# Performance work log

Hardware: AMD Instinct MI355X
Metric: run time of the kernel (lower is better)

Reference implementation:

```python
import jax, jax.numpy as jnp
import numpy as np

VOCAB = 100000
N_BLOCKS = 4
BLOCK_SIZES = [(25000, 64), (25000, 128), (25000, 256), (25000, 512)]
OUT_DIM = 512
B, L = 8, 2048


def setup_inputs() -> dict:
    key = jax.random.key(0)
    ks = jax.random.split(key, 2 * N_BLOCKS + 1)
    src = jax.random.randint(ks[0], (B, L), 0, VOCAB, dtype=jnp.int64 if jax.config.jax_enable_x64 else jnp.int32).astype(jnp.int32)
    # deterministic assignment: vocab idx -> block idx % 4, local row idx // 4
    idx = jnp.arange(VOCAB, dtype=jnp.int32)
    block_assignment = idx % N_BLOCKS
    local_assignment = idx // N_BLOCKS
    inp = {"src": src, "block_assignment": block_assignment, "local_assignment": local_assignment}
    for b, (num, size) in enumerate(BLOCK_SIZES):
        # embedding_initializer: normal_ (std=1); transformer_initializer: xavier_uniform_
        inp[f"block{b}"] = jax.random.normal(ks[1 + b], (num, size), dtype=jnp.float32)
        bound = np.sqrt(6.0 / (size + OUT_DIM))
        inp[f"trans{b}"] = jax.random.uniform(ks[1 + N_BLOCKS + b], (size, OUT_DIM), dtype=jnp.float32, minval=-bound, maxval=bound)
    return inp


def reference(src, block_assignment, local_assignment, block0, block1, block2, block3, trans0, trans1, trans2, trans3):
    blocks = [block0, block1, block2, block3]
    transformers = [trans0, trans1, trans2, trans3]
    ba = block_assignment[src]  # [B, L] which block each token routes to
    la = local_assignment[src]  # [B, L] row within that block's table
    out = jnp.zeros(src.shape + (OUT_DIM,), dtype=block0.dtype)
    for b in range(N_BLOCKS):
        tbl, tr = blocks[b], transformers[b]
        safe_la = jnp.clip(la, 0, tbl.shape[0] - 1)
        vec = tbl[safe_la]                      # [B, L, size_b] gather
        ob = jnp.einsum('bls,sd->bld', vec, tr)  # per-block transform
        out = jnp.where((ba == b)[..., None], ob, out)
    return out
```

## Files before the change

### kernel.cpp

```cpp
#include <hip/hip_runtime.h>
#include <stdint.h>


#define OUT_DIM 512
#define TOKBITS 14
#define TOKMASK ((1 << TOKBITS) - 1)

typedef __attribute__((ext_vector_type(8))) short short8;
typedef __attribute__((ext_vector_type(4))) float floatx4;

__device__ __forceinline__ uint16_t f2bf(float f) {
    union { float f; uint32_t u; } x; x.f = f;
    uint32_t u = x.u + 0x7FFF + ((x.u >> 16) & 1);
    return (uint16_t)(u >> 16);
}

__global__ __launch_bounds__(256) void prep_bsw(
    const float* __restrict__ t0, const float* __restrict__ t1,
    const float* __restrict__ t2, const float* __restrict__ t3,
    uint16_t* __restrict__ bsw, int* __restrict__ counts) {
    if (blockIdx.x == 0 && threadIdx.x < 4) counts[threadIdx.x] = 0;
    int gid = blockIdx.x * 256 + threadIdx.x;
    const float* tr; int S; int f; uint16_t* dst;
    if (gid < 4096)       { tr = t0; S = 64;  f = gid;         dst = bsw; }
    else if (gid < 12288) { tr = t1; S = 128; f = gid - 4096;  dst = bsw + 64 * 512; }
    else if (gid < 28672) { tr = t2; S = 256; f = gid - 12288; dst = bsw + (64 + 128) * 512; }
    else if (gid < 61440) { tr = t3; S = 512; f = gid - 28672; dst = bsw + (64 + 128 + 256) * 512; }
    else return;
    const int lane = f & 63, rest = f >> 6;
    const int ksteps = S >> 5;
    const int ks = rest & (ksteps - 1), ntile = rest / ksteps;
    const int quad = lane >> 4, nl = lane & 15;
    const int n = ntile * 16 + nl, k0 = ks * 32 + quad * 8;
    short8 v;
#pragma unroll
    for (int j = 0; j < 8; ++j) v[j] = (short)f2bf(tr[(k0 + j) * OUT_DIM + n]);
    *(short8*)(dst + (size_t)f * 8) = v;
}

__global__ __launch_bounds__(256) void scatter_kernel(
    const int* __restrict__ src, const int* __restrict__ ba, const int* __restrict__ la,
    int* __restrict__ counts, int* __restrict__ lists, int n_tokens, int stride) {
    __shared__ int lc[4], gbase[4];
    const int tid = (int)threadIdx.x;
    if (tid < 4) lc[tid] = 0;
    __syncthreads();
    const int t = blockIdx.x * 256 + tid;
    int b = 0, pos = 0, packed = 0;
    const bool active = (t < n_tokens);
    if (active) {
        int v = src[t];
        b = ba[v];
        int r = min(max(la[v], 0), 24999);
        packed = t | (r << TOKBITS);
        pos = atomicAdd(&lc[b], 1);
    }
    __syncthreads();
    if (tid < 4) gbase[tid] = atomicAdd(&counts[tid], lc[tid]);
    __syncthreads();
    if (active) lists[b * stride + gbase[b] + pos] = packed;
}

template <int S>
__device__ __forceinline__ void gemm3_body(
    const float* __restrict__ tbl, const uint16_t* __restrict__ bswb,
    const int* __restrict__ list, int n, int g, int nhalf,
    float* __restrict__ out, uint16_t* lds) {
    const int base = g * 16;
    const int m = min(16, n - base);
    const int tid = (int)threadIdx.x;
    constexpr int SP = S + 8;
    constexpr int CH = S / 4;
    constexpr int KS = S / 32;

    for (int i = tid; i < 16 * CH; i += 256) {
        const int row = i / CH, c = i & (CH - 1);
        float4 v = make_float4(0.f, 0.f, 0.f, 0.f);
        if (row < m) {
            const int r = list[base + row] >> TOKBITS;
            v = ((const float4*)(tbl + (size_t)r * S))[c];
        }
        const uint32_t lo = ((uint32_t)f2bf(v.y) << 16) | f2bf(v.x);
        const uint32_t hi = ((uint32_t)f2bf(v.w) << 16) | f2bf(v.z);
        *(uint2*)(lds + row * SP + c * 4) = make_uint2(lo, hi);
    }
    __syncthreads();

    const int wave = tid >> 6, lane = tid & 63;
    const int quad = lane >> 4, ml = lane & 15;
    const int ntb = nhalf * 16 + wave * 4;

    floatx4 acc[4];
#pragma unroll
    for (int nt = 0; nt < 4; ++nt) acc[nt] = (floatx4)0.f;

    const short8* B = (const short8*)bswb;
#pragma unroll
    for (int ks = 0; ks < KS; ++ks) {
        const short8 a = *(const short8*)(lds + ml * SP + ks * 32 + quad * 8);
#pragma unroll
        for (int nt = 0; nt < 4; ++nt) {
            const short8 bf = B[(size_t)((ntb + nt) * KS + ks) * 64 + lane];
            acc[nt] = __builtin_amdgcn_mfma_f32_16x16x32_bf16(a, bf, acc[nt], 0, 0, 0);
        }
    }

#pragma unroll
    for (int r = 0; r < 4; ++r) {
        const int tokidx = quad * 4 + r;
        if (tokidx < m) {
            const int t = list[base + tokidx] & TOKMASK;
            float* op = out + (size_t)t * OUT_DIM + nhalf * 256 + wave * 64 + ml;
#pragma unroll
            for (int nt = 0; nt < 4; ++nt) op[nt * 16] = acc[nt][r];
        }
    }
}

__global__ __launch_bounds__(256, 6) void gemm_mfma_v3(
    const float* __restrict__ b0, const float* __restrict__ b1,
    const float* __restrict__ b2, const float* __restrict__ b3,
    const uint16_t* __restrict__ bsw,
    const int* __restrict__ lists, const int* __restrict__ counts,
    float* __restrict__ out, int stride) {
    extern __shared__ uint16_t lds[];
    const int c0 = counts[0], c1 = counts[1], c2 = counts[2], c3 = counts[3];
    const int g0 = (c0 + 15) >> 4, g1 = (c1 + 15) >> 4, g2 = (c2 + 15) >> 4, g3 = (c3 + 15) >> 4;
    const int flat = (int)blockIdx.x;
    const int nhalf = (int)blockIdx.y;
    if (flat >= g0 + g1 + g2 + g3) return;
    if (flat < g0) {
        gemm3_body<64 >(b0, bsw, lists + 0L * stride, c0, flat, nhalf, out, lds);
    } else if (flat < g0 + g1) {
        gemm3_body<128>(b1, bsw + 64 * 512, lists + 1L * stride, c1, flat - g0, nhalf, out, lds);
    } else if (flat < g0 + g1 + g2) {
        gemm3_body<256>(b2, bsw + (64 + 128) * 512, lists + 2L * stride, c2, flat - g0 - g1, nhalf, out, lds);
    } else {
        gemm3_body<512>(b3, bsw + (64 + 128 + 256) * 512, lists + 3L * stride, c3, flat - g0 - g1 - g2, nhalf, out, lds);
    }
}

#define TOK 16
template <int S>
__device__ __forceinline__ void gemm_body(const float* __restrict__ tbl,
                                          const float* __restrict__ tr,
                                          const int* __restrict__ list,
                                          const int* __restrict__ counts,
                                          float* __restrict__ out,
                                          float* lvec, int b) {
    const int n = counts[b];
    const int base = (int)blockIdx.x * TOK;
    if (base >= n) return;
    const int m = min(TOK, n - base);
    const int tid = (int)threadIdx.x;
    const int nch = TOK * S / 4;
    for (int i = tid; i < nch; i += 256) {
        const int tok = i / (S / 4), c = i % (S / 4);
        float4 v = make_float4(0.f, 0.f, 0.f, 0.f);
        if (tok < m) {
            const int row = list[base + tok] >> TOKBITS;
            v = ((const float4*)(tbl + (size_t)row * S))[c];
        }
        ((float4*)lvec)[i] = v;
    }
    __syncthreads();
    float acc0[TOK], acc1[TOK];
#pragma unroll
    for (int tok = 0; tok < TOK; ++tok) { acc0[tok] = 0.f; acc1[tok] = 0.f; }
#pragma unroll 2
    for (int k = 0; k < S; k += 4) {
        float w00 = tr[(k + 0) * OUT_DIM + tid], w01 = tr[(k + 0) * OUT_DIM + tid + 256];
        float w10 = tr[(k + 1) * OUT_DIM + tid], w11 = tr[(k + 1) * OUT_DIM + tid + 256];
        float w20 = tr[(k + 2) * OUT_DIM + tid], w21 = tr[(k + 2) * OUT_DIM + tid + 256];
        float w30 = tr[(k + 3) * OUT_DIM + tid], w31 = tr[(k + 3) * OUT_DIM + tid + 256];
#pragma unroll
        for (int tok = 0; tok < TOK; ++tok) {
            float4 tv = *(const float4*)&lvec[tok * S + k];
            acc0[tok] += tv.x * w00 + tv.y * w10 + tv.z * w20 + tv.w * w30;
            acc1[tok] += tv.x * w01 + tv.y * w11 + tv.z * w21 + tv.w * w31;
        }
    }
    for (int tok = 0; tok < m; ++tok) {
        const int t = list[base + tok] & TOKMASK;
        out[(size_t)t * OUT_DIM + tid] = acc0[tok];
        out[(size_t)t * OUT_DIM + tid + 256] = acc1[tok];
    }
}

__global__ __launch_bounds__(256) void gemm_all(
    const float* __restrict__ b0, const float* __restrict__ b1,
    const float* __restrict__ b2, const float* __restrict__ b3,
    const float* __restrict__ t0, const float* __restrict__ t1,
    const float* __restrict__ t2, const float* __restrict__ t3,
    const int* __restrict__ lists, const int* __restrict__ counts,
    float* __restrict__ out, int stride) {
    extern __shared__ float lvec[];
    switch ((int)blockIdx.y) {
        case 0: gemm_body<64 >(b0, t0, lists + 0L * stride, counts, out, lvec, 0); break;
        case 1: gemm_body<128>(b1, t1, lists + 1L * stride, counts, out, lvec, 1); break;
        case 2: gemm_body<256>(b2, t2, lists + 2L * stride, counts, out, lvec, 2); break;
        case 3: gemm_body<512>(b3, t3, lists + 3L * stride, counts, out, lvec, 3); break;
    }
}

__global__ __launch_bounds__(256) void per_token_kernel(
    const int* __restrict__ src, const int* __restrict__ ba, const int* __restrict__ la,
    const float* __restrict__ b0, const float* __restrict__ b1,
    const float* __restrict__ b2, const float* __restrict__ b3,
    const float* __restrict__ t0, const float* __restrict__ t1,
    const float* __restrict__ t2, const float* __restrict__ t3,
    float* __restrict__ out) {
    __shared__ float lvec[OUT_DIM];
    const int t = (int)blockIdx.x, tid = (int)threadIdx.x;
    const int v = src[t];
    const int b = ba[v];
    int r = min(max(la[v], 0), 24999);
    const float* tbl; const float* tr; int S;
    switch (b) {
        case 0: tbl = b0; tr = t0; S = 64;  break;
        case 1: tbl = b1; tr = t1; S = 128; break;
        case 2: tbl = b2; tr = t2; S = 256; break;
        default: tbl = b3; tr = t3; S = 512; break;
    }
    if (tid < S / 4) ((float4*)lvec)[tid] = ((const float4*)(tbl + (size_t)r * S))[tid];
    __syncthreads();
    float acc0 = 0.f, acc1 = 0.f;
    for (int k = 0; k < S; ++k) {
        float x = lvec[k];
        acc0 += x * tr[k * OUT_DIM + tid];
        acc1 += x * tr[k * OUT_DIM + tid + 256];
    }
    out[(size_t)t * OUT_DIM + tid] = acc0;
    out[(size_t)t * OUT_DIM + tid + 256] = acc1;
}

extern "C" void kernel_launch(void* const* d_in, const int* in_sizes, int n_in,
                              void* d_out, int out_size, void* d_ws, size_t ws_size,
                              hipStream_t stream) {
    const int*   src = (const int*)d_in[0];
    const int*   ba  = (const int*)d_in[1];
    const int*   la  = (const int*)d_in[2];
    const float* b0  = (const float*)d_in[3];
    const float* t0  = (const float*)d_in[4];
    const float* b1  = (const float*)d_in[5];
    const float* t1  = (const float*)d_in[6];
    const float* b2  = (const float*)d_in[7];
    const float* t2  = (const float*)d_in[8];
    const float* b3  = (const float*)d_in[9];
    const float* t3  = (const float*)d_in[10];
    float* out = (float*)d_out;

    const int n_tokens = in_sizes[0];
    const size_t off_lists = 16;
    const size_t off_bsw   = off_lists + (size_t)4 * n_tokens * sizeof(int);
    const size_t bsw_bytes = (size_t)(64 + 128 + 256 + 512) * 512 * sizeof(uint16_t);
    const size_t need_full = off_bsw + bsw_bytes;
    const size_t need_fp32 = off_bsw;

    if (d_ws != nullptr && ws_size >= need_full) {
        int* counts   = (int*)d_ws;
        int* lists    = (int*)((char*)d_ws + off_lists);
        uint16_t* bsw = (uint16_t*)((char*)d_ws + off_bsw);
        prep_bsw<<<240, 256, 0, stream>>>(t0, t1, t2, t3, bsw, counts);
        scatter_kernel<<<(n_tokens + 255) / 256, 256, 0, stream>>>(
            src, ba, la, counts, lists, n_tokens, n_tokens);
        const int gmax = (n_tokens + 15) / 16 + 3;
        dim3 grid(gmax, 2);
        gemm_mfma_v3<<<grid, 256, 16 * (512 + 8) * sizeof(uint16_t), stream>>>(
            b0, b1, b2, b3, bsw, lists, counts, out, n_tokens);
    } else if (d_ws != nullptr && ws_size >= need_fp32) {
        int* counts = (int*)d_ws;
        int* lists  = (int*)((char*)d_ws + off_lists);
        hipMemsetAsync(d_ws, 0, 16, stream);
        scatter_kernel<<<(n_tokens + 255) / 256, 256, 0, stream>>>(
            src, ba, la, counts, lists, n_tokens, n_tokens);
        const int groups = (n_tokens + TOK - 1) / TOK;
        dim3 grid(groups, 4);
        gemm_all<<<grid, 256, TOK * OUT_DIM * sizeof(float), stream>>>(
            b0, b1, b2, b3, t0, t1, t2, t3, lists, counts, out, n_tokens);
    } else {
        per_token_kernel<<<n_tokens, 256, 0, stream>>>(
            src, ba, la, b0, b1, b2, b3, t0, t1, t2, t3, out);
    }
}
```

Measured before the change: 156.5 us.

## Fuse weight prep with token scatter and tile two M-tiles for small blocks

Merges the weight swizzle and the token scatter into one launch, with counts zeroed by a memset instead of inside the kernel. The MFMA GEMM now processes 32 tokens per workgroup for the 64- and 128-wide blocks, so each B fragment load feeds two MFMAs. Outputs are written with nontemporal stores. The trade-offs are an extra memset call, more registers (launch bound lowered to 5 waves), and the LDS size must still cover 32 rows of the smaller blocks.

```diff
diff --git a/kernel.cpp b/kernel.cpp
--- a/kernel.cpp
+++ b/kernel.cpp
@@ -15,29 +15,144 @@
     return (uint16_t)(u >> 16);
 }
 
-__global__ __launch_bounds__(256) void prep_bsw(
+__global__ __launch_bounds__(256) void prep_scatter(
     const float* __restrict__ t0, const float* __restrict__ t1,
     const float* __restrict__ t2, const float* __restrict__ t3,
-    uint16_t* __restrict__ bsw, int* __restrict__ counts) {
-    if (blockIdx.x == 0 && threadIdx.x < 4) counts[threadIdx.x] = 0;
-    int gid = blockIdx.x * 256 + threadIdx.x;
-    const float* tr; int S; int f; uint16_t* dst;
-    if (gid < 4096)       { tr = t0; S = 64;  f = gid;         dst = bsw; }
-    else if (gid < 12288) { tr = t1; S = 128; f = gid - 4096;  dst = bsw + 64 * 512; }
-    else if (gid < 28672) { tr = t2; S = 256; f = gid - 12288; dst = bsw + (64 + 128) * 512; }
-    else if (gid < 61440) { tr = t3; S = 512; f = gid - 28672; dst = bsw + (64 + 128 + 256) * 512; }
-    else return;
-    const int lane = f & 63, rest = f >> 6;
-    const int ksteps = S >> 5;
-    const int ks = rest & (ksteps - 1), ntile = rest / ksteps;
-    const int quad = lane >> 4, nl = lane & 15;
-    const int n = ntile * 16 + nl, k0 = ks * 32 + quad * 8;
-    short8 v;
-#pragma unroll
-    for (int j = 0; j < 8; ++j) v[j] = (short)f2bf(tr[(k0 + j) * OUT_DIM + n]);
-    *(short8*)(dst + (size_t)f * 8) = v;
-}
-
+    uint16_t* __restrict__ bsw,
+    const int* __restrict__ src, const int* __restrict__ ba, const int* __restrict__ la,
+    int* __restrict__ counts, int* __restrict__ lists, int n_tokens, int stride) {
+    const int bx = (int)blockIdx.x;
+    const int tid = (int)threadIdx.x;
+    if (bx < 240) {
+        int gid = bx * 256 + tid;
+        const float* tr; int S; int f; uint16_t* dst;
+        if (gid < 4096)       { tr = t0; S = 64;  f = gid;         dst = bsw; }
+        else if (gid < 12288) { tr = t1; S = 128; f = gid - 4096;  dst = bsw + 64 * 512; }
+        else if (gid < 28672) { tr = t2; S = 256; f = gid - 12288; dst = bsw + (64 + 128) * 512; }
+        else                  { tr = t3; S = 512; f = gid - 28672; dst = bsw + (64 + 128 + 256) * 512; }
+        const int lane = f & 63, rest = f >> 6;
+        const int ksteps = S >> 5;
+        const int ks = rest & (ksteps - 1), ntile = rest / ksteps;
+        const int quad = lane >> 4, nl = lane & 15;
+        const int n = ntile * 16 + nl, k0 = ks * 32 + quad * 8;
+        short8 v;
+#pragma unroll
+        for (int j = 0; j < 8; ++j) v[j] = (short)f2bf(tr[(k0 + j) * OUT_DIM + n]);
+        *(short8*)(dst + (size_t)f * 8) = v;
+    } else {
+        __shared__ int lc[4], gbase[4];
+        if (tid < 4) lc[tid] = 0;
+        __syncthreads();
+        const int t = (bx - 240) * 256 + tid;
+        int b = 0, pos = 0, packed = 0;
+        const bool active = (t < n_tokens);
+        if (active) {
+            int v = src[t];
+            b = ba[v];
+            int r = min(max(la[v], 0), 24999);
+            packed = t | (r << TOKBITS);
+            pos = atomicAdd(&lc[b], 1);
+        }
+        __syncthreads();
+        if (tid < 4) gbase[tid] = atomicAdd(&counts[tid], lc[tid]);
+        __syncthreads();
+        if (active) lists[b * stride + gbase[b] + pos] = packed;
+    }
+}
+
+template <int S, int MT>
+__device__ __forceinline__ void gemm4_body(
+    const float* __restrict__ tbl, const uint16_t* __restrict__ bswb,
+    const int* __restrict__ list, int n, int g, int nhalf,
+    float* __restrict__ out, uint16_t* lds) {
+    constexpr int ROWS = MT * 16;
+    const int base = g * ROWS;
+    const int m = min(ROWS, n - base);
+    const int tid = (int)threadIdx.x;
+    constexpr int SP = S + 8;
+    constexpr int CH = S / 4;
+    constexpr int KS = S / 32;
+
+    for (int i = tid; i < ROWS * CH; i += 256) {
+        const int row = i / CH, c = i & (CH - 1);
+        float4 v = make_float4(0.f, 0.f, 0.f, 0.f);
+        if (row < m) {
+            const int r = list[base + row] >> TOKBITS;
+            v = ((const float4*)(tbl + (size_t)r * S))[c];
+        }
+        const uint32_t lo = ((uint32_t)f2bf(v.y) << 16) | f2bf(v.x);
+        const uint32_t hi = ((uint32_t)f2bf(v.w) << 16) | f2bf(v.z);
+        *(uint2*)(lds + row * SP + c * 4) = make_uint2(lo, hi);
+    }
+    __syncthreads();
+
+    const int wave = tid >> 6, lane = tid & 63;
+    const int quad = lane >> 4, ml = lane & 15;
+    const int ntb = nhalf * 16 + wave * 4;
+
+    floatx4 acc[MT][4];
+#pragma unroll
+    for (int mt = 0; mt < MT; ++mt)
+#pragma unroll
+        for (int nt = 0; nt < 4; ++nt) acc[mt][nt] = (floatx4)0.f;
+
+    const short8* B = (const short8*)bswb;
+#pragma unroll
+    for (int ks = 0; ks < KS; ++ks) {
+        short8 a[MT];
+#pragma unroll
+        for (int mt = 0; mt < MT; ++mt)
+            a[mt] = *(const short8*)(lds + (mt * 16 + ml) * SP + ks * 32 + quad * 8);
+#pragma unroll
+        for (int nt = 0; nt < 4; ++nt) {
+            const short8 bf = B[(size_t)((ntb + nt) * KS + ks) * 64 + lane];
+#pragma unroll
+            for (int mt = 0; mt < MT; ++mt)
+                acc[mt][nt] = __builtin_amdgcn_mfma_f32_16x16x32_bf16(a[mt], bf, acc[mt][nt], 0, 0, 0);
+        }
+    }
+
+#pragma unroll
+    for (int mt = 0; mt < MT; ++mt) {
+#pragma unroll
+        for (int r = 0; r < 4; ++r) {
+            const int tokidx = mt * 16 + quad * 4 + r;
+            if (tokidx < m) {
+                const int t = list[base + tokidx] & TOKMASK;
+                float* op = out + (size_t)t * OUT_DIM + nhalf * 256 + wave * 64 + ml;
+#pragma unroll
+                for (int nt = 0; nt < 4; ++nt)
+                    __builtin_nontemporal_store(acc[mt][nt][r], op + nt * 16);
+            }
+        }
+    }
+}
+
+__global__ __launch_bounds__(256, 5) void gemm_mfma_v4(
+    const float* __restrict__ b0, const float* __restrict__ b1,
+    const float* __restrict__ b2, const float* __restrict__ b3,
+    const uint16_t* __restrict__ bsw,
+    const int* __restrict__ lists, const int* __restrict__ counts,
+    float* __restrict__ out, int stride) {
+    extern __shared__ uint16_t lds[];
+    const int c0 = counts[0], c1 = counts[1], c2 = counts[2], c3 = counts[3];
+    const int g0 = (c0 + 31) >> 5, g1 = (c1 + 31) >> 5;
+    const int g2 = (c2 + 15) >> 4, g3 = (c3 + 15) >> 4;
+    const int flat = (int)blockIdx.x;
+    const int nhalf = (int)blockIdx.y;
+    if (flat >= g0 + g1 + g2 + g3) return;
+    if (flat < g0) {
+        gemm4_body<64, 2>(b0, bsw, lists + 0L * stride, c0, flat, nhalf, out, lds);
+    } else if (flat < g0 + g1) {
+        gemm4_body<128, 2>(b1, bsw + 64 * 512, lists + 1L * stride, c1, flat - g0, nhalf, out, lds);
+    } else if (flat < g0 + g1 + g2) {
+        gemm4_body<256, 1>(b2, bsw + (64 + 128) * 512, lists + 2L * stride, c2, flat - g0 - g1, nhalf, out, lds);
+    } else {
+        gemm4_body<512, 1>(b3, bsw + (64 + 128 + 256) * 512, lists + 3L * stride, c3, flat - g0 - g1 - g2, nhalf, out, lds);
+    }
+}
+
+#define TOK 16
 __global__ __launch_bounds__(256) void scatter_kernel(
     const int* __restrict__ src, const int* __restrict__ ba, const int* __restrict__ la,
     int* __restrict__ counts, int* __restrict__ lists, int n_tokens, int stride) {
@@ -61,86 +176,6 @@
     if (active) lists[b * stride + gbase[b] + pos] = packed;
 }
 
-template <int S>
-__device__ __forceinline__ void gemm3_body(
-    const float* __restrict__ tbl, const uint16_t* __restrict__ bswb,
-    const int* __restrict__ list, int n, int g, int nhalf,
-    float* __restrict__ out, uint16_t* lds) {
-    const int base = g * 16;
-    const int m = min(16, n - base);
-    const int tid = (int)threadIdx.x;
-    constexpr int SP = S + 8;
-    constexpr int CH = S / 4;
-    constexpr int KS = S / 32;
-
-    for (int i = tid; i < 16 * CH; i += 256) {
-        const int row = i / CH, c = i & (CH - 1);
-        float4 v = make_float4(0.f, 0.f, 0.f, 0.f);
-        if (row < m) {
-            const int r = list[base + row] >> TOKBITS;
-            v = ((const float4*)(tbl + (size_t)r * S))[c];
-        }
-        const uint32_t lo = ((uint32_t)f2bf(v.y) << 16) | f2bf(v.x);
-        const uint32_t hi = ((uint32_t)f2bf(v.w) << 16) | f2bf(v.z);
-        *(uint2*)(lds + row * SP + c * 4) = make_uint2(lo, hi);
-    }
-    __syncthreads();
-
-    const int wave = tid >> 6, lane = tid & 63;
-    const int quad = lane >> 4, ml = lane & 15;
-    const int ntb = nhalf * 16 + wave * 4;
-
-    floatx4 acc[4];
-#pragma unroll
-    for (int nt = 0; nt < 4; ++nt) acc[nt] = (floatx4)0.f;
-
-    const short8* B = (const short8*)bswb;
-#pragma unroll
-    for (int ks = 0; ks < KS; ++ks) {
-        const short8 a = *(const short8*)(lds + ml * SP + ks * 32 + quad * 8);
-#pragma unroll
-        for (int nt = 0; nt < 4; ++nt) {
-            const short8 bf = B[(size_t)((ntb + nt) * KS + ks) * 64 + lane];
-            acc[nt] = __builtin_amdgcn_mfma_f32_16x16x32_bf16(a, bf, acc[nt], 0, 0, 0);
-        }
-    }
-
-#pragma unroll
-    for (int r = 0; r < 4; ++r) {
-        const int tokidx = quad * 4 + r;
-        if (tokidx < m) {
-            const int t = list[base + tokidx] & TOKMASK;
-            float* op = out + (size_t)t * OUT_DIM + nhalf * 256 + wave * 64 + ml;
-#pragma unroll
-            for (int nt = 0; nt < 4; ++nt) op[nt * 16] = acc[nt][r];
-        }
-    }
-}
-
-__global__ __launch_bounds__(256, 6) void gemm_mfma_v3(
-    const float* __restrict__ b0, const float* __restrict__ b1,
-    const float* __restrict__ b2, const float* __restrict__ b3,
-    const uint16_t* __restrict__ bsw,
-    const int* __restrict__ lists, const int* __restrict__ counts,
-    float* __restrict__ out, int stride) {
-    extern __shared__ uint16_t lds[];
-    const int c0 = counts[0], c1 = counts[1], c2 = counts[2], c3 = counts[3];
-    const int g0 = (c0 + 15) >> 4, g1 = (c1 + 15) >> 4, g2 = (c2 + 15) >> 4, g3 = (c3 + 15) >> 4;
-    const int flat = (int)blockIdx.x;
-    const int nhalf = (int)blockIdx.y;
-    if (flat >= g0 + g1 + g2 + g3) return;
-    if (flat < g0) {
-        gemm3_body<64 >(b0, bsw, lists + 0L * stride, c0, flat, nhalf, out, lds);
-    } else if (flat < g0 + g1) {
-        gemm3_body<128>(b1, bsw + 64 * 512, lists + 1L * stride, c1, flat - g0, nhalf, out, lds);
-    } else if (flat < g0 + g1 + g2) {
-        gemm3_body<256>(b2, bsw + (64 + 128) * 512, lists + 2L * stride, c2, flat - g0 - g1, nhalf, out, lds);
-    } else {
-        gemm3_body<512>(b3, bsw + (64 + 128 + 256) * 512, lists + 3L * stride, c3, flat - g0 - g1 - g2, nhalf, out, lds);
-    }
-}
-
-#define TOK 16
 template <int S>
 __device__ __forceinline__ void gemm_body(const float* __restrict__ tbl,
                                           const float* __restrict__ tr,
@@ -261,12 +296,13 @@
         int* counts   = (int*)d_ws;
         int* lists    = (int*)((char*)d_ws + off_lists);
         uint16_t* bsw = (uint16_t*)((char*)d_ws + off_bsw);
-        prep_bsw<<<240, 256, 0, stream>>>(t0, t1, t2, t3, bsw, counts);
-        scatter_kernel<<<(n_tokens + 255) / 256, 256, 0, stream>>>(
-            src, ba, la, counts, lists, n_tokens, n_tokens);
+        hipMemsetAsync(d_ws, 0, 16, stream);
+        const int scatter_wgs = (n_tokens + 255) / 256;
+        prep_scatter<<<240 + scatter_wgs, 256, 0, stream>>>(
+            t0, t1, t2, t3, bsw, src, ba, la, counts, lists, n_tokens, n_tokens);
         const int gmax = (n_tokens + 15) / 16 + 3;
         dim3 grid(gmax, 2);
-        gemm_mfma_v3<<<grid, 256, 16 * (512 + 8) * sizeof(uint16_t), stream>>>(
+        gemm_mfma_v4<<<grid, 256, 16 * (512 + 8) * sizeof(uint16_t), stream>>>(
             b0, b1, b2, b3, bsw, lists, counts, out, n_tokens);
     } else if (d_ws != nullptr && ws_size >= need_fp32) {
         int* counts = (int*)d_ws;
```

New measurement: 153.0 us (median of 2 runs). 1.02x faster.
